# Performance work log

Measured on AMD Instinct MI355X. Metric: run time of the kernel, lower is better.

The kernel has to match this reference:

```python
import jax, jax.numpy as jnp
import numpy as np

# Model config (mirrors Mamba2Block(dim=256) with mamba_ssm defaults)
D_MODEL = 256
EXPAND = 2
D_INNER = D_MODEL * EXPAND          # 512
HEADDIM = D_MODEL * EXPAND // 8     # 64
NHEADS = D_INNER // HEADDIM         # 8
D_STATE = 64
D_CONV = 4
CONV_DIM = D_INNER + 2 * D_STATE    # 640 (ngroups=1)
D_IN_PROJ = 2 * D_INNER + 2 * D_STATE + NHEADS  # 1160
BATCH, SEQLEN = 2, 2048
EPS = 1e-5


def setup_inputs() -> dict:
    key = jax.random.key(0)
    ks = jax.random.split(key, 12)
    s = 0.02
    return {
        "hidden_states": jax.random.normal(ks[0], (BATCH, SEQLEN, D_MODEL), jnp.float32),
        "norm_w": jnp.ones((D_MODEL,), jnp.float32),
        "norm_b": jnp.zeros((D_MODEL,), jnp.float32),
        "W_in": jax.random.normal(ks[1], (D_MODEL, D_IN_PROJ), jnp.float32) * s,
        "conv_w": jax.random.normal(ks[2], (CONV_DIM, D_CONV), jnp.float32) * 0.25,
        "conv_b": jnp.zeros((CONV_DIM,), jnp.float32),
        "dt_bias": jax.random.uniform(ks[3], (NHEADS,), jnp.float32),
        "A_log": jax.random.uniform(ks[4], (NHEADS,), jnp.float32),  # A = -exp(A_log) in (-e, -1]
        "D_param": jnp.ones((NHEADS,), jnp.float32),
        "rms_w": jnp.ones((D_INNER,), jnp.float32),
        "W_out": jax.random.normal(ks[5], (D_INNER, D_MODEL), jnp.float32) * s,
    }


def _layer_norm(x, w, b):
    mu = jnp.mean(x, -1, keepdims=True)
    var = jnp.mean((x - mu) ** 2, -1, keepdims=True)
    return (x - mu) * jax.lax.rsqrt(var + EPS) * w + b


def _causal_depthwise_conv(x, w, b):
    # x: [B,L,C], w: [C,K] depthwise causal conv
    B, L, C = x.shape
    K = w.shape[1]
    xp = jnp.pad(x, ((0, 0), (K - 1, 0), (0, 0)))
    y = b
    for k in range(K):  # K=4, fixed small kernel
        y = y + w[:, k] * xp[:, k:k + L, :]
    return y


def reference(hidden_states, norm_w, norm_b, W_in, conv_w, conv_b, dt_bias, A_log, D_param, rms_w, W_out):
    B, L, D = hidden_states.shape
    residual = hidden_states                       # residual is None, drop_path=0
    x = _layer_norm(residual, norm_w, norm_b)      # pre-norm

    zxbcdt = jnp.einsum("bld,de->ble", x, W_in)    # [B,L,2*Di+2*N+H]
    z = zxbcdt[..., :D_INNER]
    xBC = zxbcdt[..., D_INNER:D_INNER + CONV_DIM]
    dt = zxbcdt[..., -NHEADS:]

    xBC = jax.nn.silu(_causal_depthwise_conv(xBC, conv_w, conv_b))
    xs = xBC[..., :D_INNER]
    Bm = xBC[..., D_INNER:D_INNER + D_STATE]       # [B,L,N] (ngroups=1)
    Cm = xBC[..., D_INNER + D_STATE:]              # [B,L,N]

    dt = jax.nn.softplus(dt + dt_bias)             # [B,L,H]
    A = -jnp.exp(A_log)                            # [H]
    dA = jnp.exp(dt * A)                           # [B,L,H]

    xh = xs.reshape(B, L, NHEADS, HEADDIM)         # [B,L,H,P]
    dtx = dt[..., None] * xh                       # [B,L,H,P]

    def step(s, inp):
        dA_t, dtx_t, B_t, C_t = inp                # [B,H],[B,H,P],[B,N],[B,N]
        s = s * dA_t[:, :, None, None] + dtx_t[..., None] * B_t[:, None, None, :]
        y_t = jnp.einsum("bhpn,bn->bhp", s, C_t)
        return s, y_t

    s0 = jnp.zeros((B, NHEADS, HEADDIM, D_STATE), hidden_states.dtype)
    xs_in = (jnp.swapaxes(dA, 0, 1), jnp.swapaxes(dtx, 0, 1),
             jnp.swapaxes(Bm, 0, 1), jnp.swapaxes(Cm, 0, 1))
    _, ys = jax.lax.scan(step, s0, xs_in)          # ys: [L,B,H,P]
    y = jnp.swapaxes(ys, 0, 1) + D_param[None, None, :, None] * xh  # skip term
    y = y.reshape(B, L, D_INNER)

    # gated RMSNorm (norm_before_gate=False): rmsnorm(y * silu(z)) * rms_w
    g = y * jax.nn.silu(z)
    g = g * jax.lax.rsqrt(jnp.mean(g * g, -1, keepdims=True) + EPS) * rms_w

    out = jnp.einsum("bld,de->ble", g, W_out)
    return out, residual
```

## Files before the change

kernel.cpp:

```cpp
#include <hip/hip_runtime.h>
#include <hip/hip_bf16.h>

#define BATCH 2
#define SEQLEN 2048
#define DMODEL 256
#define DINNER 512
#define NHEADS 8
#define HEADDIM 64
#define DSTATE 64
#define CONVDIM 640
#define DINPROJ 1160
#define NTOK (BATCH*SEQLEN)
#define Q 64
#define NCH (SEQLEN/Q)
#define NPAD_IN 1216
#define TS 72
#define RS2 198

typedef short v8s __attribute__((ext_vector_type(8)));
typedef float v4f __attribute__((ext_vector_type(4)));

__device__ __forceinline__ unsigned short f2bf(float f){
    __hip_bfloat16 h = __float2bfloat16(f);
    return *reinterpret_cast<unsigned short*>(&h);
}
__device__ __forceinline__ float bf2f(unsigned short u){
    unsigned int x = ((unsigned int)u) << 16;
    return __uint_as_float(x);
}

__global__ __launch_bounds__(256) void k_ln(
        const float* __restrict__ hid, const float* __restrict__ nw, const float* __restrict__ nb,
        float* __restrict__ res, unsigned short* __restrict__ Xb){
    __shared__ float xs[16][DMODEL];
    int t = threadIdx.x, tok0 = blockIdx.x*16;
    for(int i=0;i<16;i++){
        int idx = i*256+t; int j = idx>>8, c = idx&255;
        float v = hid[(size_t)(tok0+j)*DMODEL + c];
        xs[j][c] = v;
        res[(size_t)(tok0+j)*DMODEL + c] = v;
    }
    __syncthreads();
    int g = t>>4, il = t&15;
    float sum=0.f, sumsq=0.f;
    for(int i=0;i<16;i++){ float v = xs[g][il*16+i]; sum += v; sumsq += v*v; }
    #pragma unroll
    for(int m=1;m<16;m<<=1){ sum += __shfl_xor(sum,m); sumsq += __shfl_xor(sumsq,m); }
    float mu   = sum*(1.f/256.f);
    float var  = sumsq*(1.f/256.f) - mu*mu;
    float rstd = rsqrtf(var + 1e-5f);
    for(int i=0;i<16;i++){
        int c = il*16+i;
        xs[g][c] = (xs[g][c]-mu)*rstd*nw[c] + nb[c];
    }
    __syncthreads();
    for(int i=0;i<16;i++){
        int idx = i*256+t; int j = idx>>8, c = idx&255;
        Xb[(size_t)(tok0+j)*DMODEL + c] = f2bf(xs[j][c]);
    }
}

__global__ __launch_bounds__(256) void k_cvt(const float* __restrict__ Win, const float* __restrict__ Wout,
                                             unsigned short* __restrict__ Wti, unsigned short* __restrict__ Wto){
    int bx = blockIdx.x;
    if(bx < NPAD_IN/4){
        int n0 = bx*4, k = threadIdx.x;
        #pragma unroll
        for(int i=0;i<4;i++){
            int n = n0+i;
            float v = (n < DINPROJ) ? Win[(size_t)k*DINPROJ + n] : 0.f;
            Wti[(size_t)n*DMODEL + k] = f2bf(v);
        }
    } else {
        int n0 = (bx - NPAD_IN/4)*4;
        #pragma unroll
        for(int kk=0;kk<2;kk++){
            int k = threadIdx.x + kk*256;
            #pragma unroll
            for(int i=0;i<4;i++){
                int n = n0+i;
                Wto[(size_t)n*DINNER + k] = f2bf(Wout[(size_t)k*DMODEL + n]);
            }
        }
    }
}

template<int BF16OUT>
__global__ __launch_bounds__(256) void k_gemm(
        const unsigned short* __restrict__ A, const unsigned short* __restrict__ Bt,
        float* __restrict__ Cf, unsigned short* __restrict__ Cb, int K, int Ncols){
    __shared__ __align__(16) unsigned short As[128*40];
    __shared__ __align__(16) unsigned short Bs[64*40];
    int t = threadIdx.x;
    int lane = t & 63, w = t >> 6;
    int lanelow = lane & 15, quad = lane >> 4;
    int tok0 = blockIdx.x * 128;
    int n0   = blockIdx.y * 64;
    v4f acc[2][4];
    #pragma unroll
    for(int mi=0;mi<2;mi++)
        #pragma unroll
        for(int ni=0;ni<4;ni++)
            acc[mi][ni] = (v4f){0.f,0.f,0.f,0.f};
    for(int k0=0; k0<K; k0+=32){
        __syncthreads();
        #pragma unroll
        for(int cc=0; cc<2; cc++){
            int c = t + cc*256;
            int row = c>>2, off = c&3;
            uint4 v = *(const uint4*)(A + (size_t)(tok0+row)*K + k0 + off*8);
            *(uint4*)&As[row*40 + off*8] = v;
        }
        {
            int row = t>>2, off = t&3;
            uint4 v = *(const uint4*)(Bt + (size_t)(n0+row)*K + k0 + off*8);
            *(uint4*)&Bs[row*40 + off*8] = v;
        }
        __syncthreads();
        v8s a0 = *(const v8s*)&As[(w*32 +      lanelow)*40 + quad*8];
        v8s a1 = *(const v8s*)&As[(w*32 + 16 + lanelow)*40 + quad*8];
        v8s b[4];
        #pragma unroll
        for(int ni=0;ni<4;ni++)
            b[ni] = *(const v8s*)&Bs[(ni*16 + lanelow)*40 + quad*8];
        #pragma unroll
        for(int ni=0;ni<4;ni++){
            acc[0][ni] = __builtin_amdgcn_mfma_f32_16x16x32_bf16(a0, b[ni], acc[0][ni], 0,0,0);
            acc[1][ni] = __builtin_amdgcn_mfma_f32_16x16x32_bf16(a1, b[ni], acc[1][ni], 0,0,0);
        }
    }
    #pragma unroll
    for(int mi=0;mi<2;mi++){
        #pragma unroll
        for(int ni=0;ni<4;ni++){
            int col = n0 + ni*16 + lanelow;
            if(col < Ncols){
                #pragma unroll
                for(int r=0;r<4;r++){
                    int row = tok0 + w*32 + mi*16 + quad*4 + r;
                    if(BF16OUT) Cb[(size_t)row*Ncols + col] = f2bf(acc[mi][ni][r]);
                    else        Cf[(size_t)row*Ncols + col] = acc[mi][ni][r];
                }
            }
        }
    }
}

__global__ __launch_bounds__(256) void k_chunk1(
        const unsigned short* __restrict__ zxb, const float* __restrict__ conv_w, const float* __restrict__ conv_b,
        const float* __restrict__ dt_bias, const float* __restrict__ A_log, const float* __restrict__ D_param,
        unsigned short* __restrict__ yw16, float* __restrict__ contrib,
        float* __restrict__ Larr, float* __restrict__ decayArr, unsigned short* __restrict__ Ccv){
    int blk = blockIdx.x;
    int c = blk & 31, h = (blk>>5)&7, b = blk>>8;
    int t = threadIdx.x;
    int lane = t & 63, w = t >> 6;
    int lanelow = lane & 15, quad = lane >> 4;
    __shared__ __align__(16) unsigned short raw[67*RS2];
    __shared__ __align__(16) unsigned short Cb[64*TS];
    __shared__ __align__(16) unsigned short Bb[64*TS];
    __shared__ __align__(16) unsigned short BtW[64*TS];
    __shared__ __align__(16) unsigned short Xt[64*TS];
    __shared__ float Ls[Q], dts[Q], wch[Q];
    unsigned short* Gbuf = raw;
    int l0 = c*Q;
    int bh = b*NHEADS + h;
    const unsigned short* zbase = zxb + (size_t)(b*SEQLEN + l0)*DINPROJ;
    for(int i=0;i<7;i++){
        int gidx = t + 256*i;
        if(gidx < 67*24){
            int row = gidx/24, g = gidx%24;
            int ltok = l0 - 3 + row;
            int gcol = (g<8) ? (DINNER + h*HEADDIM + g*8) : (2*DINNER + (g-8)*8);
            uint4 v;
            if(ltok >= 0) v = *(const uint4*)(zbase + (ptrdiff_t)(row-3)*DINPROJ + gcol);
            else { v.x=0; v.y=0; v.z=0; v.w=0; }
            int ch = (g<8) ? g*8 : 64 + (g-8)*8;
            unsigned int* d = (unsigned int*)&raw[row*RS2 + ch];
            d[0]=v.x; d[1]=v.y; d[2]=v.z; d[3]=v.w;
        }
    }
    if(t < Q){
        float v = bf2f(zbase[(size_t)t*DINPROJ + (DINPROJ-NHEADS) + h]) + dt_bias[h];
        float dt = (v > 20.f) ? v : log1pf(__expf(v));
        float A  = -__expf(A_log[h]);
        float ld = dt*A;
        #pragma unroll
        for(int off=1; off<64; off<<=1){
            float u = __shfl_up(ld, off);
            if(lane >= off) ld += u;
        }
        Ls[t] = ld; dts[t] = dt;
    }
    __syncthreads();
    float L63 = Ls[Q-1];
    if(t < Q) wch[t] = __expf(L63 - Ls[t]) * dts[t];
    __syncthreads();
    unsigned short* CcP = Ccv + ((size_t)b*NCH + c)*4096;
    for(int i=0;i<12;i++){
        int u = t + 256*i;
        int st = u & 63, c4 = u >> 6, ch = c4*4;
        float xk[4][4];
        #pragma unroll
        for(int k=0;k<4;k++){
            const unsigned short* rp = &raw[(st+k)*RS2 + ch];
            ushort2 p0 = *(const ushort2*)rp;
            ushort2 p1 = *(const ushort2*)(rp+2);
            xk[k][0]=bf2f(p0.x); xk[k][1]=bf2f(p0.y); xk[k][2]=bf2f(p1.x); xk[k][3]=bf2f(p1.y);
        }
        float wst = wch[st];
        #pragma unroll
        for(int j=0;j<4;j++){
            int chj = ch+j;
            int cc = (chj<64) ? (h*HEADDIM + chj) : (448 + chj);
            float4 wv = *(const float4*)&conv_w[cc*4];
            float acc = conv_b[cc] + wv.x*xk[0][j] + wv.y*xk[1][j] + wv.z*xk[2][j] + wv.w*xk[3][j];
            float sv = acc/(1.f+__expf(-acc));
            if(chj < 64){
                Xt[chj*TS + st] = f2bf(sv);
            } else if(chj < 128){
                int n = chj-64;
                Bb[st*TS + n]  = f2bf(sv);
                BtW[n*TS + st] = f2bf(sv*wst);
            } else {
                int n = chj-128;
                unsigned short sb = f2bf(sv);
                Cb[st*TS + n] = sb;
                if(h==0) CcP[st*64 + n] = sb;
            }
        }
    }
    __syncthreads();
    v4f g[4];
    #pragma unroll
    for(int nt=0;nt<4;nt++) g[nt] = (v4f){0.f,0.f,0.f,0.f};
    #pragma unroll
    for(int kk=0;kk<2;kk++){
        v8s a = *(const v8s*)&Cb[(w*16+lanelow)*TS + kk*32 + quad*8];
        #pragma unroll
        for(int nt=0;nt<4;nt++){
            v8s bb = *(const v8s*)&Bb[(nt*16+lanelow)*TS + kk*32 + quad*8];
            g[nt] = __builtin_amdgcn_mfma_f32_16x16x32_bf16(a, bb, g[nt], 0,0,0);
        }
    }
    float Lrow[4];
    #pragma unroll
    for(int r=0;r<4;r++) Lrow[r] = Ls[w*16 + quad*4 + r];
    #pragma unroll
    for(int nt=0;nt<4;nt++){
        int col = nt*16 + lanelow;
        float Lc = Ls[col], dtc = dts[col];
        #pragma unroll
        for(int r=0;r<4;r++){
            int rowg = w*16 + quad*4 + r;
            float val = (col <= rowg) ? g[nt][r] * __expf(Lrow[r]-Lc) * dtc : 0.f;
            Gbuf[rowg*TS + col] = f2bf(val);
        }
    }
    __syncthreads();
    v4f ya[4], sa[4];
    #pragma unroll
    for(int nt=0;nt<4;nt++){ ya[nt]=(v4f){0.f,0.f,0.f,0.f}; sa[nt]=(v4f){0.f,0.f,0.f,0.f}; }
    #pragma unroll
    for(int kk=0;kk<2;kk++){
        v8s ag = *(const v8s*)&Gbuf[(w*16+lanelow)*TS + kk*32 + quad*8];
        v8s ax = *(const v8s*)&Xt[(w*16+lanelow)*TS + kk*32 + quad*8];
        #pragma unroll
        for(int nt=0;nt<4;nt++){
            v8s bx = *(const v8s*)&Xt[(nt*16+lanelow)*TS + kk*32 + quad*8];
            v8s bw = *(const v8s*)&BtW[(nt*16+lanelow)*TS + kk*32 + quad*8];
            ya[nt] = __builtin_amdgcn_mfma_f32_16x16x32_bf16(ag, bx, ya[nt], 0,0,0);
            sa[nt] = __builtin_amdgcn_mfma_f32_16x16x32_bf16(ax, bw, sa[nt], 0,0,0);
        }
    }
    float Dp = D_param[h];
    #pragma unroll
    for(int nt=0;nt<4;nt++){
        int col = nt*16 + lanelow;
        #pragma unroll
        for(int r=0;r<4;r++){
            int i = w*16 + quad*4 + r;
            float xval = bf2f(Xt[col*TS + i]);
            yw16[((size_t)b*SEQLEN + l0 + i)*DINNER + h*HEADDIM + col] = f2bf(ya[nt][r] + Dp*xval);
            contrib[(((size_t)bh*NCH + c)*64 + i)*64 + col] = sa[nt][r];
        }
    }
    if(t < Q) Larr[((size_t)bh*NCH + c)*Q + t] = Ls[t];
    if(t == 0) decayArr[bh*NCH + c] = __expf(L63);
}

__global__ __launch_bounds__(256) void k_chunk2(const float* __restrict__ contrib,
                                                const float* __restrict__ decayArr,
                                                unsigned short* __restrict__ Sb){
    int bh = blockIdx.x >> 4;
    int part = blockIdx.x & 15;
    int e = part*256 + threadIdx.x;
    const size_t base = (size_t)bh*NCH*4096 + e;
    float vals[NCH];
    #pragma unroll
    for(int c=0;c<NCH;c++) vals[c] = contrib[base + (size_t)c*4096];
    float s = 0.f;
    #pragma unroll
    for(int c=0;c<NCH;c++){
        Sb[base + (size_t)c*4096] = f2bf(s);
        s = fmaf(s, decayArr[bh*NCH + c], vals[c]);
    }
}

__global__ __launch_bounds__(512) void k_tail(
        const unsigned short* __restrict__ Ccv, const unsigned short* __restrict__ Sb,
        const float* __restrict__ Larr, const unsigned short* __restrict__ yw16,
        const unsigned short* __restrict__ zxb, const float* __restrict__ rms_w,
        unsigned short* __restrict__ Gb){
    int blk = blockIdx.x;
    int c = blk & 31, b = blk >> 5;
    int t = threadIdx.x;
    int h = t >> 6, lane = t & 63;
    int lanelow = lane & 15, quad = lane >> 4;
    int bh = b*NHEADS + h;
    __shared__ float wsum[8][64];
    __shared__ float rstdS[64];
    const unsigned short* Cp = Ccv + ((size_t)b*NCH + c)*4096;
    const unsigned short* Sp = Sb + ((size_t)bh*NCH + c)*4096;
    v8s a[4][2];
    #pragma unroll
    for(int rt=0;rt<4;rt++){
        a[rt][0] = *(const v8s*)(Cp + (rt*16+lanelow)*64 + quad*8);
        a[rt][1] = *(const v8s*)(Cp + (rt*16+lanelow)*64 + 32 + quad*8);
    }
    v8s s[4][2];
    #pragma unroll
    for(int nt=0;nt<4;nt++){
        s[nt][0] = *(const v8s*)(Sp + (nt*16+lanelow)*64 + quad*8);
        s[nt][1] = *(const v8s*)(Sp + (nt*16+lanelow)*64 + 32 + quad*8);
    }
    float g[4][4][4];
    float sq[4][4];
    const float* Lp = Larr + ((size_t)bh*NCH + c)*Q;
    #pragma unroll
    for(int rt=0;rt<4;rt++){
        float eL[4];
        #pragma unroll
        for(int r=0;r<4;r++) eL[r] = __expf(Lp[rt*16 + quad*4 + r]);
        #pragma unroll
        for(int nt=0;nt<4;nt++){
            v4f acc = (v4f){0.f,0.f,0.f,0.f};
            acc = __builtin_amdgcn_mfma_f32_16x16x32_bf16(a[rt][0], s[nt][0], acc, 0,0,0);
            acc = __builtin_amdgcn_mfma_f32_16x16x32_bf16(a[rt][1], s[nt][1], acc, 0,0,0);
            int col = h*HEADDIM + nt*16 + lanelow;
            #pragma unroll
            for(int r=0;r<4;r++){
                int i = rt*16 + quad*4 + r;
                size_t tok = (size_t)b*SEQLEN + c*Q + i;
                float yv = acc[r]*eL[r] + bf2f(yw16[tok*DINNER + col]);
                float z  = bf2f(zxb[tok*DINPROJ + col]);
                float gg = yv * (z/(1.f+__expf(-z)));
                g[rt][nt][r] = gg;
                sq[rt][r] = (nt==0 ? gg*gg : sq[rt][r] + gg*gg);
            }
        }
    }
    #pragma unroll
    for(int rt=0;rt<4;rt++)
        #pragma unroll
        for(int r=0;r<4;r++){
            float v = sq[rt][r];
            #pragma unroll
            for(int m=1;m<16;m<<=1) v += __shfl_xor(v, m);
            sq[rt][r] = v;
        }
    if(lanelow==0){
        #pragma unroll
        for(int rt=0;rt<4;rt++)
            #pragma unroll
            for(int r=0;r<4;r++)
                wsum[h][rt*16 + quad*4 + r] = sq[rt][r];
    }
    __syncthreads();
    if(t < 64){
        float tot = 0.f;
        #pragma unroll
        for(int hh=0;hh<8;hh++) tot += wsum[hh][t];
        rstdS[t] = rsqrtf(tot*(1.f/512.f) + 1e-5f);
    }
    __syncthreads();
    #pragma unroll
    for(int rt=0;rt<4;rt++){
        #pragma unroll
        for(int nt=0;nt<4;nt++){
            int col = h*HEADDIM + nt*16 + lanelow;
            float rw = rms_w[col];
            #pragma unroll
            for(int r=0;r<4;r++){
                int i = rt*16 + quad*4 + r;
                Gb[((size_t)b*SEQLEN + c*Q + i)*DINNER + col] = f2bf(g[rt][nt][r] * rstdS[i] * rw);
            }
        }
    }
}

extern "C" void kernel_launch(void* const* d_in, const int* in_sizes, int n_in,
                              void* d_out, int out_size, void* d_ws, size_t ws_size,
                              hipStream_t stream) {
    const float* hid     = (const float*)d_in[0];
    const float* norm_w  = (const float*)d_in[1];
    const float* norm_b  = (const float*)d_in[2];
    const float* Win     = (const float*)d_in[3];
    const float* conv_w  = (const float*)d_in[4];
    const float* conv_b  = (const float*)d_in[5];
    const float* dt_bias = (const float*)d_in[6];
    const float* A_log   = (const float*)d_in[7];
    const float* D_param = (const float*)d_in[8];
    const float* rms_w   = (const float*)d_in[9];
    const float* Wout    = (const float*)d_in[10];

    float* ws = (float*)d_ws;
    float* contrib = ws;
    float* Larr    = contrib + (size_t)16*NCH*4096;
    float* decayA  = Larr + (size_t)16*NCH*Q;
    unsigned short* zxb  = (unsigned short*)(decayA + 512);
    unsigned short* yw16 = zxb + (size_t)NTOK*DINPROJ;
    unsigned short* Sb   = yw16 + (size_t)NTOK*DINNER;
    unsigned short* Ccv  = Sb + (size_t)16*NCH*4096;
    unsigned short* Xb   = Ccv + (size_t)BATCH*NCH*4096;
    unsigned short* Gb   = Xb + (size_t)NTOK*DMODEL;
    unsigned short* Wti  = Gb + (size_t)NTOK*DINNER;
    unsigned short* Wto  = Wti + (size_t)NPAD_IN*DMODEL;

    float* out = (float*)d_out;
    float* res = out + (size_t)NTOK*DMODEL;

    k_ln<<<NTOK/16, 256, 0, stream>>>(hid, norm_w, norm_b, res, Xb);
    k_cvt<<<NPAD_IN/4 + DMODEL/4, 256, 0, stream>>>(Win, Wout, Wti, Wto);
    k_gemm<1><<<dim3(NTOK/128, NPAD_IN/64), 256, 0, stream>>>(Xb, Wti, nullptr, zxb, DMODEL, DINPROJ);
    k_chunk1<<<BATCH*NHEADS*NCH, 256, 0, stream>>>(zxb, conv_w, conv_b, dt_bias, A_log, D_param,
                                                   yw16, contrib, Larr, decayA, Ccv);
    k_chunk2<<<256, 256, 0, stream>>>(contrib, decayA, Sb);
    k_tail<<<BATCH*NCH, 512, 0, stream>>>(Ccv, Sb, Larr, yw16, zxb, rms_w, Gb);
    k_gemm<0><<<dim3(NTOK/128, DMODEL/64), 256, 0, stream>>>(Gb, Wto, out, nullptr, DINNER, DMODEL);
}
```

Measured before the change: 150.3 us.

## Merge LN and weight-convert kernels, read conv inputs directly, split tail blocks

Merges the layernorm and weight-conversion kernels into one launch, which saves one kernel launch. In chunk1 the shared-memory staging of the conv input window is removed, and each thread instead reads its four taps directly from global memory. This frees LDS, since Gbuf now gets its own buffer, but it brings redundant global loads. The tail kernel is split into two half-chunk blocks per chunk, which doubles the grid from 64 to 128 blocks for better CU occupancy.

```diff
diff --git a/kernel.cpp b/kernel.cpp
--- a/kernel.cpp
+++ b/kernel.cpp
@@ -15,7 +15,6 @@
 #define NCH (SEQLEN/Q)
 #define NPAD_IN 1216
 #define TS 72
-#define RS2 198
 
 typedef short v8s __attribute__((ext_vector_type(8)));
 typedef float v4f __attribute__((ext_vector_type(4)));
@@ -29,42 +28,42 @@
     return __uint_as_float(x);
 }
 
-__global__ __launch_bounds__(256) void k_ln(
+__global__ __launch_bounds__(256) void k_prep(
         const float* __restrict__ hid, const float* __restrict__ nw, const float* __restrict__ nb,
-        float* __restrict__ res, unsigned short* __restrict__ Xb){
-    __shared__ float xs[16][DMODEL];
-    int t = threadIdx.x, tok0 = blockIdx.x*16;
-    for(int i=0;i<16;i++){
-        int idx = i*256+t; int j = idx>>8, c = idx&255;
-        float v = hid[(size_t)(tok0+j)*DMODEL + c];
-        xs[j][c] = v;
-        res[(size_t)(tok0+j)*DMODEL + c] = v;
-    }
-    __syncthreads();
-    int g = t>>4, il = t&15;
-    float sum=0.f, sumsq=0.f;
-    for(int i=0;i<16;i++){ float v = xs[g][il*16+i]; sum += v; sumsq += v*v; }
-    #pragma unroll
-    for(int m=1;m<16;m<<=1){ sum += __shfl_xor(sum,m); sumsq += __shfl_xor(sumsq,m); }
-    float mu   = sum*(1.f/256.f);
-    float var  = sumsq*(1.f/256.f) - mu*mu;
-    float rstd = rsqrtf(var + 1e-5f);
-    for(int i=0;i<16;i++){
-        int c = il*16+i;
-        xs[g][c] = (xs[g][c]-mu)*rstd*nw[c] + nb[c];
-    }
-    __syncthreads();
-    for(int i=0;i<16;i++){
-        int idx = i*256+t; int j = idx>>8, c = idx&255;
-        Xb[(size_t)(tok0+j)*DMODEL + c] = f2bf(xs[j][c]);
-    }
-}
-
-__global__ __launch_bounds__(256) void k_cvt(const float* __restrict__ Win, const float* __restrict__ Wout,
-                                             unsigned short* __restrict__ Wti, unsigned short* __restrict__ Wto){
+        const float* __restrict__ Win, const float* __restrict__ Wout,
+        float* __restrict__ res, unsigned short* __restrict__ Xb,
+        unsigned short* __restrict__ Wti, unsigned short* __restrict__ Wto){
     int bx = blockIdx.x;
-    if(bx < NPAD_IN/4){
-        int n0 = bx*4, k = threadIdx.x;
+    int t = threadIdx.x;
+    if(bx < 256){
+        __shared__ float xs[16][DMODEL];
+        int tok0 = bx*16;
+        for(int i=0;i<16;i++){
+            int idx = i*256+t; int j = idx>>8, c = idx&255;
+            float v = hid[(size_t)(tok0+j)*DMODEL + c];
+            xs[j][c] = v;
+            res[(size_t)(tok0+j)*DMODEL + c] = v;
+        }
+        __syncthreads();
+        int g = t>>4, il = t&15;
+        float sum=0.f, sumsq=0.f;
+        for(int i=0;i<16;i++){ float v = xs[g][il*16+i]; sum += v; sumsq += v*v; }
+        #pragma unroll
+        for(int m=1;m<16;m<<=1){ sum += __shfl_xor(sum,m); sumsq += __shfl_xor(sumsq,m); }
+        float mu   = sum*(1.f/256.f);
+        float var  = sumsq*(1.f/256.f) - mu*mu;
+        float rstd = rsqrtf(var + 1e-5f);
+        for(int i=0;i<16;i++){
+            int c = il*16+i;
+            xs[g][c] = (xs[g][c]-mu)*rstd*nw[c] + nb[c];
+        }
+        __syncthreads();
+        for(int i=0;i<16;i++){
+            int idx = i*256+t; int j = idx>>8, c = idx&255;
+            Xb[(size_t)(tok0+j)*DMODEL + c] = f2bf(xs[j][c]);
+        }
+    } else if(bx < 256 + NPAD_IN/4){
+        int n0 = (bx-256)*4, k = t;
         #pragma unroll
         for(int i=0;i<4;i++){
             int n = n0+i;
@@ -72,10 +71,10 @@
             Wti[(size_t)n*DMODEL + k] = f2bf(v);
         }
     } else {
-        int n0 = (bx - NPAD_IN/4)*4;
+        int n0 = (bx - 256 - NPAD_IN/4)*4;
         #pragma unroll
         for(int kk=0;kk<2;kk++){
-            int k = threadIdx.x + kk*256;
+            int k = t + kk*256;
             #pragma unroll
             for(int i=0;i<4;i++){
                 int n = n0+i;
@@ -156,30 +155,15 @@
     int t = threadIdx.x;
     int lane = t & 63, w = t >> 6;
     int lanelow = lane & 15, quad = lane >> 4;
-    __shared__ __align__(16) unsigned short raw[67*RS2];
     __shared__ __align__(16) unsigned short Cb[64*TS];
     __shared__ __align__(16) unsigned short Bb[64*TS];
     __shared__ __align__(16) unsigned short BtW[64*TS];
     __shared__ __align__(16) unsigned short Xt[64*TS];
+    __shared__ __align__(16) unsigned short Gbuf[64*TS];
     __shared__ float Ls[Q], dts[Q], wch[Q];
-    unsigned short* Gbuf = raw;
     int l0 = c*Q;
     int bh = b*NHEADS + h;
     const unsigned short* zbase = zxb + (size_t)(b*SEQLEN + l0)*DINPROJ;
-    for(int i=0;i<7;i++){
-        int gidx = t + 256*i;
-        if(gidx < 67*24){
-            int row = gidx/24, g = gidx%24;
-            int ltok = l0 - 3 + row;
-            int gcol = (g<8) ? (DINNER + h*HEADDIM + g*8) : (2*DINNER + (g-8)*8);
-            uint4 v;
-            if(ltok >= 0) v = *(const uint4*)(zbase + (ptrdiff_t)(row-3)*DINPROJ + gcol);
-            else { v.x=0; v.y=0; v.z=0; v.w=0; }
-            int ch = (g<8) ? g*8 : 64 + (g-8)*8;
-            unsigned int* d = (unsigned int*)&raw[row*RS2 + ch];
-            d[0]=v.x; d[1]=v.y; d[2]=v.z; d[3]=v.w;
-        }
-    }
     if(t < Q){
         float v = bf2f(zbase[(size_t)t*DINPROJ + (DINPROJ-NHEADS) + h]) + dt_bias[h];
         float dt = (v > 20.f) ? v : log1pf(__expf(v));
@@ -200,13 +184,16 @@
     for(int i=0;i<12;i++){
         int u = t + 256*i;
         int st = u & 63, c4 = u >> 6, ch = c4*4;
+        int gcol = (ch < 64) ? (DINNER + h*HEADDIM + ch) : (2*DINNER + (ch-64));
+        const unsigned short* colp = zbase + (ptrdiff_t)st*DINPROJ + gcol;
         float xk[4][4];
         #pragma unroll
         for(int k=0;k<4;k++){
-            const unsigned short* rp = &raw[(st+k)*RS2 + ch];
-            ushort2 p0 = *(const ushort2*)rp;
-            ushort2 p1 = *(const ushort2*)(rp+2);
-            xk[k][0]=bf2f(p0.x); xk[k][1]=bf2f(p0.y); xk[k][2]=bf2f(p1.x); xk[k][3]=bf2f(p1.y);
+            int l = l0 + st + k - 3;
+            ushort4 v;
+            if(l >= 0) v = *(const ushort4*)(colp - (ptrdiff_t)(3-k)*DINPROJ);
+            else { v.x=0; v.y=0; v.z=0; v.w=0; }
+            xk[k][0]=bf2f(v.x); xk[k][1]=bf2f(v.y); xk[k][2]=bf2f(v.z); xk[k][3]=bf2f(v.w);
         }
         float wst = wch[st];
         #pragma unroll
@@ -313,20 +300,21 @@
         const unsigned short* __restrict__ zxb, const float* __restrict__ rms_w,
         unsigned short* __restrict__ Gb){
     int blk = blockIdx.x;
-    int c = blk & 31, b = blk >> 5;
+    int half = blk & 1, c = (blk>>1) & 31, b = blk >> 6;
     int t = threadIdx.x;
     int h = t >> 6, lane = t & 63;
     int lanelow = lane & 15, quad = lane >> 4;
     int bh = b*NHEADS + h;
-    __shared__ float wsum[8][64];
-    __shared__ float rstdS[64];
+    __shared__ float wsum[8][32];
+    __shared__ float rstdS[32];
     const unsigned short* Cp = Ccv + ((size_t)b*NCH + c)*4096;
     const unsigned short* Sp = Sb + ((size_t)bh*NCH + c)*4096;
-    v8s a[4][2];
-    #pragma unroll
-    for(int rt=0;rt<4;rt++){
-        a[rt][0] = *(const v8s*)(Cp + (rt*16+lanelow)*64 + quad*8);
-        a[rt][1] = *(const v8s*)(Cp + (rt*16+lanelow)*64 + 32 + quad*8);
+    v8s a[2][2];
+    #pragma unroll
+    for(int rt=0;rt<2;rt++){
+        int row = half*32 + rt*16 + lanelow;
+        a[rt][0] = *(const v8s*)(Cp + row*64 + quad*8);
+        a[rt][1] = *(const v8s*)(Cp + row*64 + 32 + quad*8);
     }
     v8s s[4][2];
     #pragma unroll
@@ -334,14 +322,14 @@
         s[nt][0] = *(const v8s*)(Sp + (nt*16+lanelow)*64 + quad*8);
         s[nt][1] = *(const v8s*)(Sp + (nt*16+lanelow)*64 + 32 + quad*8);
     }
-    float g[4][4][4];
-    float sq[4][4];
+    float g[2][4][4];
+    float sq[2][4];
     const float* Lp = Larr + ((size_t)bh*NCH + c)*Q;
     #pragma unroll
-    for(int rt=0;rt<4;rt++){
+    for(int rt=0;rt<2;rt++){
         float eL[4];
         #pragma unroll
-        for(int r=0;r<4;r++) eL[r] = __expf(Lp[rt*16 + quad*4 + r]);
+        for(int r=0;r<4;r++) eL[r] = __expf(Lp[half*32 + rt*16 + quad*4 + r]);
         #pragma unroll
         for(int nt=0;nt<4;nt++){
             v4f acc = (v4f){0.f,0.f,0.f,0.f};
@@ -350,7 +338,7 @@
             int col = h*HEADDIM + nt*16 + lanelow;
             #pragma unroll
             for(int r=0;r<4;r++){
-                int i = rt*16 + quad*4 + r;
+                int i = half*32 + rt*16 + quad*4 + r;
                 size_t tok = (size_t)b*SEQLEN + c*Q + i;
                 float yv = acc[r]*eL[r] + bf2f(yw16[tok*DINNER + col]);
                 float z  = bf2f(zxb[tok*DINPROJ + col]);
@@ -361,7 +349,7 @@
         }
     }
     #pragma unroll
-    for(int rt=0;rt<4;rt++)
+    for(int rt=0;rt<2;rt++)
         #pragma unroll
         for(int r=0;r<4;r++){
             float v = sq[rt][r];
@@ -371,13 +359,13 @@
         }
     if(lanelow==0){
         #pragma unroll
-        for(int rt=0;rt<4;rt++)
+        for(int rt=0;rt<2;rt++)
             #pragma unroll
             for(int r=0;r<4;r++)
                 wsum[h][rt*16 + quad*4 + r] = sq[rt][r];
     }
     __syncthreads();
-    if(t < 64){
+    if(t < 32){
         float tot = 0.f;
         #pragma unroll
         for(int hh=0;hh<8;hh++) tot += wsum[hh][t];
@@ -385,7 +373,7 @@
     }
     __syncthreads();
     #pragma unroll
-    for(int rt=0;rt<4;rt++){
+    for(int rt=0;rt<2;rt++){
         #pragma unroll
         for(int nt=0;nt<4;nt++){
             int col = h*HEADDIM + nt*16 + lanelow;
@@ -393,7 +381,7 @@
             #pragma unroll
             for(int r=0;r<4;r++){
                 int i = rt*16 + quad*4 + r;
-                Gb[((size_t)b*SEQLEN + c*Q + i)*DINNER + col] = f2bf(g[rt][nt][r] * rstdS[i] * rw);
+                Gb[((size_t)b*SEQLEN + c*Q + half*32 + i)*DINNER + col] = f2bf(g[rt][nt][r] * rstdS[i] * rw);
             }
         }
     }
@@ -430,12 +418,11 @@
     float* out = (float*)d_out;
     float* res = out + (size_t)NTOK*DMODEL;
 
-    k_ln<<<NTOK/16, 256, 0, stream>>>(hid, norm_w, norm_b, res, Xb);
-    k_cvt<<<NPAD_IN/4 + DMODEL/4, 256, 0, stream>>>(Win, Wout, Wti, Wto);
+    k_prep<<<256 + NPAD_IN/4 + DMODEL/4, 256, 0, stream>>>(hid, norm_w, norm_b, Win, Wout, res, Xb, Wti, Wto);
     k_gemm<1><<<dim3(NTOK/128, NPAD_IN/64), 256, 0, stream>>>(Xb, Wti, nullptr, zxb, DMODEL, DINPROJ);
     k_chunk1<<<BATCH*NHEADS*NCH, 256, 0, stream>>>(zxb, conv_w, conv_b, dt_bias, A_log, D_param,
                                                    yw16, contrib, Larr, decayA, Ccv);
     k_chunk2<<<256, 256, 0, stream>>>(contrib, decayA, Sb);
-    k_tail<<<BATCH*NCH, 512, 0, stream>>>(Ccv, Sb, Larr, yw16, zxb, rms_w, Gb);
+    k_tail<<<BATCH*NCH*2, 512, 0, stream>>>(Ccv, Sb, Larr, yw16, zxb, rms_w, Gb);
     k_gemm<0><<<dim3(NTOK/128, DMODEL/64), 256, 0, stream>>>(Gb, Wto, out, nullptr, DINNER, DMODEL);
 }
```

New measurement: 146.3 us. 1.03x faster.
